# Kernel tuning notes

Measured on AMD Instinct MI355X. Metric: run time of the kernel, lower is better.

The kernel has to match this reference:

```python
import jax, jax.numpy as jnp
import numpy as np

def setup_inputs() -> dict:
    key = jax.random.key(0)
    ks = jax.random.split(key, 6)
    ch, cr = 256, 32  # cr = ch // 8
    B, H, W = 4, 64, 64
    sc = 1.0 / np.sqrt(ch)
    return {
        "inputs": jax.random.normal(ks[0], (B, H, W, ch), jnp.float32),
        "Wf": jax.random.normal(ks[1], (ch, cr), jnp.float32) * sc,
        "bf": jnp.zeros((cr,), jnp.float32),
        "Wg": jax.random.normal(ks[2], (ch, cr), jnp.float32) * sc,
        "bg": jnp.zeros((cr,), jnp.float32),
        "Wh": jax.random.normal(ks[3], (ch, cr), jnp.float32) * sc,
        "bh": jnp.zeros((cr,), jnp.float32),
        "Wv": jax.random.normal(ks[4], (cr, ch), jnp.float32) * (1.0 / np.sqrt(cr)),
        "bv": jnp.zeros((ch,), jnp.float32),
        "gamma": jnp.zeros((1,), jnp.float32),
    }

def reference(inputs, Wf, bf, Wg, bg, Wh, bh, Wv, bv, gamma):
    B, H, W, C = inputs.shape
    x = inputs.reshape(B, H * W, C)  # [B, N, C]
    f = x @ Wf + bf  # [B, N, cr] (keys)
    g = x @ Wg + bg  # [B, N, cr] (queries)
    h = x @ Wh + bh  # [B, N, cr] (values)
    s = jnp.einsum('bnk,bmk->bnm', g, f)  # [B, N, N]
    beta = jax.nn.softmax(s, axis=-1)
    v = jnp.einsum('bnm,bmk->bnk', beta, h)  # [B, N, cr]
    o = v @ Wv + bv  # [B, N, C]
    out = gamma * o + x
    return out.reshape(B, H, W, C)
```

## Files before the change

kernel.cpp:

```cpp
#include <hip/hip_runtime.h>

#define B_SZ  4
#define N_TOK 4096
#define CH    256
#define CR    32
#define SEG   512
#define KT    64
#define NITER (SEG / KT)
#define LOG2E 1.44269504f
#define SHIFT2 (12.0f * 1.44269504f)

typedef __attribute__((ext_vector_type(8))) short bf16x8;
typedef __attribute__((ext_vector_type(4))) float f32x4;

__device__ inline ushort f2bf(float x) {
    uint u = __float_as_uint(x);
    u += 0x7fff + ((u >> 16) & 1);
    return (ushort)(u >> 16);
}
__device__ inline uint pk2bf(float a, float b) {
    return __builtin_amdgcn_perm(__float_as_uint(b), __float_as_uint(a), 0x07060302);
}
__device__ inline float fast_exp2(float x) {
#if __has_builtin(__builtin_amdgcn_exp2f)
    return __builtin_amdgcn_exp2f(x);
#else
    return exp2f(x);
#endif
}

__global__ __launch_bounds__(256) void prep_kernel(
    const float* __restrict__ Wf, const float* __restrict__ Wg,
    const float* __restrict__ Wh, const float* __restrict__ Wv,
    ushort* __restrict__ wft, ushort* __restrict__ wgt,
    ushort* __restrict__ wht, ushort* __restrict__ wvt)
{
    int t = threadIdx.x, blk = blockIdx.x;
    if (blk < 3) {
        const float* W  = (blk == 0) ? Wf : (blk == 1) ? Wg : Wh;
        ushort*      Wt = (blk == 0) ? wft : (blk == 1) ? wgt : wht;
        int j = t & 31, half = t >> 5;
        ushort tmp[32];
        #pragma unroll
        for (int kk = 0; kk < 32; ++kk)
            tmp[kk] = f2bf(W[(half * 32 + kk) * CR + j]);
        ushort* dst = Wt + (size_t)j * CH + half * 32;
        #pragma unroll
        for (int k8 = 0; k8 < 4; ++k8)
            *(bf16x8*)(dst + k8 * 8) = *(bf16x8*)&tmp[k8 * 8];
    } else {
        ushort tmp[32];
        #pragma unroll
        for (int k = 0; k < CR; ++k) tmp[k] = f2bf(Wv[k * CH + t]);
        ushort* dst = wvt + (size_t)t * CR;
        #pragma unroll
        for (int k8 = 0; k8 < 4; ++k8)
            *(bf16x8*)(dst + k8 * 8) = *(bf16x8*)&tmp[k8 * 8];
    }
}

__global__ __launch_bounds__(256) void proj_kernel(
    const float* __restrict__ x,
    const ushort* __restrict__ wft, const ushort* __restrict__ wgt, const ushort* __restrict__ wht,
    const float* __restrict__ bf_, const float* __restrict__ bg, const float* __restrict__ bh,
    ushort* __restrict__ fo, ushort* __restrict__ go, ushort* __restrict__ hto)
{
    __shared__ f32x4 accx[3][6][64];
    int t  = threadIdx.x;
    int wv = t >> 6, L = t & 63, nl = L & 15, Q = L >> 4;
    int row_t = blockIdx.x * 16;
    int b = row_t >> 12, tok0 = row_t & 4095;

    const float* xrow = x + (size_t)(row_t + nl) * CH;
    f32x4 A[6];
    #pragma unroll
    for (int i = 0; i < 6; ++i) A[i] = (f32x4){0.f, 0.f, 0.f, 0.f};

    #pragma unroll
    for (int c2 = 0; c2 < 2; ++c2) {
        int off = wv * 64 + c2 * 32 + Q * 8;
        float4 lo = *(const float4*)(xrow + off);
        float4 hi = *(const float4*)(xrow + off + 4);
        bf16x8 xa;
        xa[0] = (short)f2bf(lo.x); xa[1] = (short)f2bf(lo.y);
        xa[2] = (short)f2bf(lo.z); xa[3] = (short)f2bf(lo.w);
        xa[4] = (short)f2bf(hi.x); xa[5] = (short)f2bf(hi.y);
        xa[6] = (short)f2bf(hi.z); xa[7] = (short)f2bf(hi.w);

        bf16x8 wf0 = *(const bf16x8*)(wft + (size_t)nl * CH + off);
        bf16x8 wf1 = *(const bf16x8*)(wft + (size_t)(16 + nl) * CH + off);
        bf16x8 wg0 = *(const bf16x8*)(wgt + (size_t)nl * CH + off);
        bf16x8 wg1 = *(const bf16x8*)(wgt + (size_t)(16 + nl) * CH + off);
        bf16x8 wh0 = *(const bf16x8*)(wht + (size_t)nl * CH + off);
        bf16x8 wh1 = *(const bf16x8*)(wht + (size_t)(16 + nl) * CH + off);

        A[0] = __builtin_amdgcn_mfma_f32_16x16x32_bf16(xa, wf0, A[0], 0, 0, 0);
        A[1] = __builtin_amdgcn_mfma_f32_16x16x32_bf16(xa, wf1, A[1], 0, 0, 0);
        A[2] = __builtin_amdgcn_mfma_f32_16x16x32_bf16(xa, wg0, A[2], 0, 0, 0);
        A[3] = __builtin_amdgcn_mfma_f32_16x16x32_bf16(xa, wg1, A[3], 0, 0, 0);
        A[4] = __builtin_amdgcn_mfma_f32_16x16x32_bf16(wh0, xa, A[4], 0, 0, 0);
        A[5] = __builtin_amdgcn_mfma_f32_16x16x32_bf16(wh1, xa, A[5], 0, 0, 0);
    }

    if (wv > 0) {
        #pragma unroll
        for (int i = 0; i < 6; ++i) accx[wv - 1][i][L] = A[i];
    }
    __syncthreads();
    if (wv == 0) {
        #pragma unroll
        for (int i = 0; i < 6; ++i) {
            f32x4 s0 = accx[0][i][L], s1 = accx[1][i][L], s2 = accx[2][i][L];
            A[i] = A[i] + s0 + s1 + s2;
        }
        float bF0 = bf_[nl], bF1 = bf_[16 + nl];
        float bG0 = bg[nl] * LOG2E, bG1 = bg[16 + nl] * LOG2E;
        #pragma unroll
        for (int r = 0; r < 4; ++r) {
            size_t ro = (size_t)(row_t + Q * 4 + r) * CR;
            fo[ro + nl]      = f2bf(A[0][r] + bF0);
            fo[ro + 16 + nl] = f2bf(A[1][r] + bF1);
            go[ro + nl]      = f2bf(fmaf(A[2][r], LOG2E, bG0));
            go[ro + 16 + nl] = f2bf(fmaf(A[3][r], LOG2E, bG1));
        }
        ushort* hb = hto + (size_t)b * CR * N_TOK + tok0 + nl;
        #pragma unroll
        for (int r = 0; r < 4; ++r) {
            int ch = Q * 4 + r;
            hb[(size_t)ch * N_TOK]        = f2bf(A[4][r] + bh[ch]);
            hb[(size_t)(16 + ch) * N_TOK] = f2bf(A[5][r] + bh[16 + ch]);
        }
    }
}

__global__ __launch_bounds__(512, 4) void attn_kernel(
    const ushort* __restrict__ f, const ushort* __restrict__ g,
    const ushort* __restrict__ ht, const ushort* __restrict__ wvt,
    const float* __restrict__ bv, const float* __restrict__ gamma,
    const float* __restrict__ x, float* __restrict__ out)
{
    __shared__ unsigned long long smem_raw[38912 / 8];
    ushort (*pls)[32][76]  = (ushort (*)[32][76])smem_raw;
    float  (*obuf)[32][33] = (float (*)[32][33])smem_raw;
    float  (*lbuf)[32]     = (float (*)[32])((char*)smem_raw + 33792);
    ushort (*oc)[48]       = (ushort (*)[48])((char*)smem_raw + 34816);

    int t  = threadIdx.x;
    int wv = t >> 6;
    int L  = t & 63;
    int nl = L & 15;
    int Q  = L >> 4;
    int b  = blockIdx.x >> 7;
    int q0 = (blockIdx.x & 127) * 32;

    const ushort* fb  = f  + (size_t)b * N_TOK * CR;
    const ushort* htb = ht + (size_t)b * CR * N_TOK;

    bf16x8 gB0 = *(const bf16x8*)(g + ((size_t)b * N_TOK + q0 + nl) * CR + Q * 8);
    bf16x8 gB1 = *(const bf16x8*)(g + ((size_t)b * N_TOK + q0 + 16 + nl) * CR + Q * 8);

    f32x4 acc00 = {0,0,0,0}, acc01 = {0,0,0,0};
    f32x4 acc10 = {0,0,0,0}, acc11 = {0,0,0,0};
    const f32x4 zf = {0,0,0,0};
    float lsum0 = 0.f, lsum1 = 0.f;

    int key0 = wv * SEG;
    bf16x8 Ac0 = *(const bf16x8*)(fb + (size_t)(key0 +  0 + nl) * CR + Q * 8);
    bf16x8 Ac1 = *(const bf16x8*)(fb + (size_t)(key0 + 16 + nl) * CR + Q * 8);
    bf16x8 Ac2 = *(const bf16x8*)(fb + (size_t)(key0 + 32 + nl) * CR + Q * 8);
    bf16x8 Ac3 = *(const bf16x8*)(fb + (size_t)(key0 + 48 + nl) * CR + Q * 8);

    #pragma unroll 2
    for (int it = 0; it < NITER; ++it) {
        int kc = wv * SEG + it * KT;
        const ushort* hk = htb + (size_t)nl * N_TOK + kc;
        bf16x8 b00 = *(const bf16x8*)(hk + Q * 8);
        bf16x8 b01 = *(const bf16x8*)(hk + (size_t)16 * N_TOK + Q * 8);
        bf16x8 b10 = *(const bf16x8*)(hk + 32 + Q * 8);
        bf16x8 b11 = *(const bf16x8*)(hk + (size_t)16 * N_TOK + 32 + Q * 8);
        int kn = wv * SEG + ((it + 1 < NITER) ? it + 1 : 0) * KT;
        const ushort* fn = fb + (size_t)kn * CR;
        bf16x8 An0 = *(const bf16x8*)(fn + (size_t)( 0 + nl) * CR + Q * 8);
        bf16x8 An1 = *(const bf16x8*)(fn + (size_t)(16 + nl) * CR + Q * 8);
        bf16x8 An2 = *(const bf16x8*)(fn + (size_t)(32 + nl) * CR + Q * 8);
        bf16x8 An3 = *(const bf16x8*)(fn + (size_t)(48 + nl) * CR + Q * 8);

        f32x4 s00 = __builtin_amdgcn_mfma_f32_16x16x32_bf16(Ac0, gB0, zf, 0, 0, 0);
        f32x4 s01 = __builtin_amdgcn_mfma_f32_16x16x32_bf16(Ac1, gB0, zf, 0, 0, 0);
        f32x4 s02 = __builtin_amdgcn_mfma_f32_16x16x32_bf16(Ac2, gB0, zf, 0, 0, 0);
        f32x4 s03 = __builtin_amdgcn_mfma_f32_16x16x32_bf16(Ac3, gB0, zf, 0, 0, 0);
        f32x4 s10 = __builtin_amdgcn_mfma_f32_16x16x32_bf16(Ac0, gB1, zf, 0, 0, 0);
        f32x4 s11 = __builtin_amdgcn_mfma_f32_16x16x32_bf16(Ac1, gB1, zf, 0, 0, 0);
        f32x4 s12 = __builtin_amdgcn_mfma_f32_16x16x32_bf16(Ac2, gB1, zf, 0, 0, 0);
        f32x4 s13 = __builtin_amdgcn_mfma_f32_16x16x32_bf16(Ac3, gB1, zf, 0, 0, 0);

        #pragma unroll
        for (int qh = 0; qh < 2; ++qh) {
            f32x4 v0 = qh ? s10 : s00, v1 = qh ? s11 : s01;
            f32x4 v2 = qh ? s12 : s02, v3 = qh ? s13 : s03;
            int row = qh * 16 + nl;
            float p0 = fast_exp2(v0[0]-SHIFT2), p1 = fast_exp2(v0[1]-SHIFT2);
            float p2 = fast_exp2(v0[2]-SHIFT2), p3 = fast_exp2(v0[3]-SHIFT2);
            float s4 = ((p0+p1)+(p2+p3));
            uint2 w; w.x = pk2bf(p0,p1); w.y = pk2bf(p2,p3);
            *(uint2*)&pls[wv][row][ 0 + Q * 4] = w;
            p0 = fast_exp2(v1[0]-SHIFT2); p1 = fast_exp2(v1[1]-SHIFT2);
            p2 = fast_exp2(v1[2]-SHIFT2); p3 = fast_exp2(v1[3]-SHIFT2);
            s4 += ((p0+p1)+(p2+p3));
            w.x = pk2bf(p0,p1); w.y = pk2bf(p2,p3);
            *(uint2*)&pls[wv][row][16 + Q * 4] = w;
            p0 = fast_exp2(v2[0]-SHIFT2); p1 = fast_exp2(v2[1]-SHIFT2);
            p2 = fast_exp2(v2[2]-SHIFT2); p3 = fast_exp2(v2[3]-SHIFT2);
            s4 += ((p0+p1)+(p2+p3));
            w.x = pk2bf(p0,p1); w.y = pk2bf(p2,p3);
            *(uint2*)&pls[wv][row][32 + Q * 4] = w;
            p0 = fast_exp2(v3[0]-SHIFT2); p1 = fast_exp2(v3[1]-SHIFT2);
            p2 = fast_exp2(v3[2]-SHIFT2); p3 = fast_exp2(v3[3]-SHIFT2);
            s4 += ((p0+p1)+(p2+p3));
            w.x = pk2bf(p0,p1); w.y = pk2bf(p2,p3);
            *(uint2*)&pls[wv][row][48 + Q * 4] = w;
            if (qh) lsum1 += s4; else lsum0 += s4;
        }

        bf16x8 aP00 = *(const bf16x8*)&pls[wv][     nl][ 0 + Q * 8];
        bf16x8 aP01 = *(const bf16x8*)&pls[wv][     nl][32 + Q * 8];
        bf16x8 aP10 = *(const bf16x8*)&pls[wv][16 + nl][ 0 + Q * 8];
        bf16x8 aP11 = *(const bf16x8*)&pls[wv][16 + nl][32 + Q * 8];

        acc00 = __builtin_amdgcn_mfma_f32_16x16x32_bf16(aP00, b00, acc00, 0, 0, 0);
        acc01 = __builtin_amdgcn_mfma_f32_16x16x32_bf16(aP00, b01, acc01, 0, 0, 0);
        acc10 = __builtin_amdgcn_mfma_f32_16x16x32_bf16(aP10, b00, acc10, 0, 0, 0);
        acc11 = __builtin_amdgcn_mfma_f32_16x16x32_bf16(aP10, b01, acc11, 0, 0, 0);
        acc00 = __builtin_amdgcn_mfma_f32_16x16x32_bf16(aP01, b10, acc00, 0, 0, 0);
        acc01 = __builtin_amdgcn_mfma_f32_16x16x32_bf16(aP01, b11, acc01, 0, 0, 0);
        acc10 = __builtin_amdgcn_mfma_f32_16x16x32_bf16(aP11, b10, acc10, 0, 0, 0);
        acc11 = __builtin_amdgcn_mfma_f32_16x16x32_bf16(aP11, b11, acc11, 0, 0, 0);

        Ac0 = An0; Ac1 = An1; Ac2 = An2; Ac3 = An3;
    }

    lsum0 += __shfl_xor(lsum0, 16); lsum0 += __shfl_xor(lsum0, 32);
    lsum1 += __shfl_xor(lsum1, 16); lsum1 += __shfl_xor(lsum1, 32);

    __syncthreads();
    #pragma unroll
    for (int r = 0; r < 4; ++r) {
        obuf[wv][     Q * 4 + r][nl]      = acc00[r];
        obuf[wv][     Q * 4 + r][16 + nl] = acc01[r];
        obuf[wv][16 + Q * 4 + r][nl]      = acc10[r];
        obuf[wv][16 + Q * 4 + r][16 + nl] = acc11[r];
    }
    if (L < 16) { lbuf[wv][nl] = lsum0; lbuf[wv][16 + nl] = lsum1; }
    __syncthreads();

    {
        int ch = t & 31, qb = t >> 5;
        #pragma unroll
        for (int qq = qb; qq < 32; qq += 16) {
            float s = 0.f, Lq = 0.f;
            #pragma unroll
            for (int w = 0; w < 8; ++w) { s += obuf[w][qq][ch]; Lq += lbuf[w][qq]; }
            oc[qq][ch] = f2bf(s / Lq);
        }
    }
    __syncthreads();

    bf16x8 aO0 = *(const bf16x8*)&oc[     nl][Q * 8];
    bf16x8 aO1 = *(const bf16x8*)&oc[16 + nl][Q * 8];
    float gm = gamma[0];
    const float* xb = x   + ((size_t)b * N_TOK + q0) * CH;
    float*       ob = out + ((size_t)b * N_TOK + q0) * CH;
    #pragma unroll
    for (int i = 0; i < 2; ++i) {
        int nb = wv * 2 + i;
        bf16x8 bW = *(const bf16x8*)(wvt + (size_t)(nb * 16 + nl) * CR + Q * 8);
        f32x4 d0 = __builtin_amdgcn_mfma_f32_16x16x32_bf16(aO0, bW, zf, 0, 0, 0);
        f32x4 d1 = __builtin_amdgcn_mfma_f32_16x16x32_bf16(aO1, bW, zf, 0, 0, 0);
        int c = nb * 16 + nl;
        float bvc = bv[c];
        #pragma unroll
        for (int r = 0; r < 4; ++r) {
            int qa = Q * 4 + r;
            ob[qa * CH + c]        = fmaf(gm, d0[r] + bvc, xb[qa * CH + c]);
            ob[(16 + qa) * CH + c] = fmaf(gm, d1[r] + bvc, xb[(16 + qa) * CH + c]);
        }
    }
}

extern "C" void kernel_launch(void* const* d_in, const int* in_sizes, int n_in,
                              void* d_out, int out_size, void* d_ws, size_t ws_size,
                              hipStream_t stream) {
    const float* x     = (const float*)d_in[0];
    const float* Wf    = (const float*)d_in[1];
    const float* bf_   = (const float*)d_in[2];
    const float* Wg    = (const float*)d_in[3];
    const float* bg    = (const float*)d_in[4];
    const float* Wh    = (const float*)d_in[5];
    const float* bh    = (const float*)d_in[6];
    const float* Wv    = (const float*)d_in[7];
    const float* bv    = (const float*)d_in[8];
    const float* gamma = (const float*)d_in[9];
    float* out = (float*)d_out;

    const size_t T = (size_t)B_SZ * N_TOK * CR;
    ushort* fo  = (ushort*)d_ws;
    ushort* go  = fo + T;
    ushort* hto = go + T;
    ushort* wvt = hto + T;
    ushort* wft = wvt + CH * CR;
    ushort* wgt = wft + CH * CR;
    ushort* wht = wgt + CH * CR;

    prep_kernel<<<4, 256, 0, stream>>>(Wf, Wg, Wh, Wv, wft, wgt, wht, wvt);
    proj_kernel<<<B_SZ * N_TOK / 16, 256, 0, stream>>>(x, wft, wgt, wht, bf_, bg, bh, fo, go, hto);
    attn_kernel<<<B_SZ * (N_TOK / 32), 512, 0, stream>>>(fo, go, hto, wvt, bv, gamma, x, out);
}
```

Measured before the change: 121.8 us.

## Software-pipeline QK and PV stages, compute row sums via MFMA, swizzle blocks

The attention loop is restructured so the QK^T scores and exponentials for the next key tile are computed before the PV MFMAs of the current tile. This overlaps the exp/pack work of one tile with the matrix work of another, and the PV MFMAs are raised to higher priority with s_setprio. Softmax row sums now come from extra MFMAs against a vector of ones, replacing the per-lane VALU adds and cross-lane shuffles. The constant exponent shift is removed and block indices are swizzled across batches to change cache locality. The trade-offs are more MFMA work, more live registers, and a higher overflow risk in the unshifted exponent if scores grow large.

```diff
diff --git a/kernel.cpp b/kernel.cpp
--- a/kernel.cpp
+++ b/kernel.cpp
@@ -8,7 +8,6 @@
 #define KT    64
 #define NITER (SEG / KT)
 #define LOG2E 1.44269504f
-#define SHIFT2 (12.0f * 1.44269504f)
 
 typedef __attribute__((ext_vector_type(8))) short bf16x8;
 typedef __attribute__((ext_vector_type(4))) float f32x4;
@@ -27,6 +26,13 @@
 #else
     return exp2f(x);
 #endif
+}
+
+__device__ inline void exp_pack_store(const f32x4 v, ushort* dst) {
+    float p0 = fast_exp2(v[0]), p1 = fast_exp2(v[1]);
+    float p2 = fast_exp2(v[2]), p3 = fast_exp2(v[3]);
+    uint2 w; w.x = pk2bf(p0, p1); w.y = pk2bf(p2, p3);
+    *(uint2*)dst = w;
 }
 
 __global__ __launch_bounds__(256) void prep_kernel(
@@ -150,8 +156,10 @@
     int L  = t & 63;
     int nl = L & 15;
     int Q  = L >> 4;
-    int b  = blockIdx.x >> 7;
-    int q0 = (blockIdx.x & 127) * 32;
+    int bid = blockIdx.x;
+    int swz = (bid & 7) * 64 + (bid >> 3);
+    int b  = swz >> 7;
+    int q0 = (swz & 127) * 32;
 
     const ushort* fb  = f  + (size_t)b * N_TOK * CR;
     const ushort* htb = ht + (size_t)b * CR * N_TOK;
@@ -161,72 +169,83 @@
 
     f32x4 acc00 = {0,0,0,0}, acc01 = {0,0,0,0};
     f32x4 acc10 = {0,0,0,0}, acc11 = {0,0,0,0};
+    f32x4 accS0 = {0,0,0,0}, accS1 = {0,0,0,0};
     const f32x4 zf = {0,0,0,0};
-    float lsum0 = 0.f, lsum1 = 0.f;
+
+    bf16x8 ones;
+    #pragma unroll
+    for (int i = 0; i < 8; ++i) ones[i] = (short)0x3F80;
 
     int key0 = wv * SEG;
-    bf16x8 Ac0 = *(const bf16x8*)(fb + (size_t)(key0 +  0 + nl) * CR + Q * 8);
-    bf16x8 Ac1 = *(const bf16x8*)(fb + (size_t)(key0 + 16 + nl) * CR + Q * 8);
-    bf16x8 Ac2 = *(const bf16x8*)(fb + (size_t)(key0 + 32 + nl) * CR + Q * 8);
-    bf16x8 Ac3 = *(const bf16x8*)(fb + (size_t)(key0 + 48 + nl) * CR + Q * 8);
-
-    #pragma unroll 2
+
+    bf16x8 Ap0 = *(const bf16x8*)(fb + (size_t)(key0 +  0 + nl) * CR + Q * 8);
+    bf16x8 Ap1 = *(const bf16x8*)(fb + (size_t)(key0 + 16 + nl) * CR + Q * 8);
+    bf16x8 Ap2 = *(const bf16x8*)(fb + (size_t)(key0 + 32 + nl) * CR + Q * 8);
+    bf16x8 Ap3 = *(const bf16x8*)(fb + (size_t)(key0 + 48 + nl) * CR + Q * 8);
+    bf16x8 An0 = *(const bf16x8*)(fb + (size_t)(key0 + KT +  0 + nl) * CR + Q * 8);
+    bf16x8 An1 = *(const bf16x8*)(fb + (size_t)(key0 + KT + 16 + nl) * CR + Q * 8);
+    bf16x8 An2 = *(const bf16x8*)(fb + (size_t)(key0 + KT + 32 + nl) * CR + Q * 8);
+    bf16x8 An3 = *(const bf16x8*)(fb + (size_t)(key0 + KT + 48 + nl) * CR + Q * 8);
+
+    {
+        f32x4 s0 = __builtin_amdgcn_mfma_f32_16x16x32_bf16(Ap0, gB0, zf, 0, 0, 0);
+        f32x4 s1 = __builtin_amdgcn_mfma_f32_16x16x32_bf16(Ap1, gB0, zf, 0, 0, 0);
+        f32x4 s2 = __builtin_amdgcn_mfma_f32_16x16x32_bf16(Ap2, gB0, zf, 0, 0, 0);
+        f32x4 s3 = __builtin_amdgcn_mfma_f32_16x16x32_bf16(Ap3, gB0, zf, 0, 0, 0);
+        exp_pack_store(s0, &pls[wv][nl][ 0 + Q * 4]);
+        exp_pack_store(s1, &pls[wv][nl][16 + Q * 4]);
+        exp_pack_store(s2, &pls[wv][nl][32 + Q * 4]);
+        exp_pack_store(s3, &pls[wv][nl][48 + Q * 4]);
+        s0 = __builtin_amdgcn_mfma_f32_16x16x32_bf16(Ap0, gB1, zf, 0, 0, 0);
+        s1 = __builtin_amdgcn_mfma_f32_16x16x32_bf16(Ap1, gB1, zf, 0, 0, 0);
+        s2 = __builtin_amdgcn_mfma_f32_16x16x32_bf16(Ap2, gB1, zf, 0, 0, 0);
+        s3 = __builtin_amdgcn_mfma_f32_16x16x32_bf16(Ap3, gB1, zf, 0, 0, 0);
+        exp_pack_store(s0, &pls[wv][16 + nl][ 0 + Q * 4]);
+        exp_pack_store(s1, &pls[wv][16 + nl][16 + Q * 4]);
+        exp_pack_store(s2, &pls[wv][16 + nl][32 + Q * 4]);
+        exp_pack_store(s3, &pls[wv][16 + nl][48 + Q * 4]);
+    }
+
+    #pragma unroll
     for (int it = 0; it < NITER; ++it) {
-        int kc = wv * SEG + it * KT;
+        bf16x8 aP00 = *(const bf16x8*)&pls[wv][     nl][ 0 + Q * 8];
+        bf16x8 aP01 = *(const bf16x8*)&pls[wv][     nl][32 + Q * 8];
+        bf16x8 aP10 = *(const bf16x8*)&pls[wv][16 + nl][ 0 + Q * 8];
+        bf16x8 aP11 = *(const bf16x8*)&pls[wv][16 + nl][32 + Q * 8];
+        int kc = key0 + it * KT;
         const ushort* hk = htb + (size_t)nl * N_TOK + kc;
         bf16x8 b00 = *(const bf16x8*)(hk + Q * 8);
         bf16x8 b01 = *(const bf16x8*)(hk + (size_t)16 * N_TOK + Q * 8);
         bf16x8 b10 = *(const bf16x8*)(hk + 32 + Q * 8);
         bf16x8 b11 = *(const bf16x8*)(hk + (size_t)16 * N_TOK + 32 + Q * 8);
-        int kn = wv * SEG + ((it + 1 < NITER) ? it + 1 : 0) * KT;
-        const ushort* fn = fb + (size_t)kn * CR;
-        bf16x8 An0 = *(const bf16x8*)(fn + (size_t)( 0 + nl) * CR + Q * 8);
-        bf16x8 An1 = *(const bf16x8*)(fn + (size_t)(16 + nl) * CR + Q * 8);
-        bf16x8 An2 = *(const bf16x8*)(fn + (size_t)(32 + nl) * CR + Q * 8);
-        bf16x8 An3 = *(const bf16x8*)(fn + (size_t)(48 + nl) * CR + Q * 8);
-
-        f32x4 s00 = __builtin_amdgcn_mfma_f32_16x16x32_bf16(Ac0, gB0, zf, 0, 0, 0);
-        f32x4 s01 = __builtin_amdgcn_mfma_f32_16x16x32_bf16(Ac1, gB0, zf, 0, 0, 0);
-        f32x4 s02 = __builtin_amdgcn_mfma_f32_16x16x32_bf16(Ac2, gB0, zf, 0, 0, 0);
-        f32x4 s03 = __builtin_amdgcn_mfma_f32_16x16x32_bf16(Ac3, gB0, zf, 0, 0, 0);
-        f32x4 s10 = __builtin_amdgcn_mfma_f32_16x16x32_bf16(Ac0, gB1, zf, 0, 0, 0);
-        f32x4 s11 = __builtin_amdgcn_mfma_f32_16x16x32_bf16(Ac1, gB1, zf, 0, 0, 0);
-        f32x4 s12 = __builtin_amdgcn_mfma_f32_16x16x32_bf16(Ac2, gB1, zf, 0, 0, 0);
-        f32x4 s13 = __builtin_amdgcn_mfma_f32_16x16x32_bf16(Ac3, gB1, zf, 0, 0, 0);
-
-        #pragma unroll
-        for (int qh = 0; qh < 2; ++qh) {
-            f32x4 v0 = qh ? s10 : s00, v1 = qh ? s11 : s01;
-            f32x4 v2 = qh ? s12 : s02, v3 = qh ? s13 : s03;
-            int row = qh * 16 + nl;
-            float p0 = fast_exp2(v0[0]-SHIFT2), p1 = fast_exp2(v0[1]-SHIFT2);
-            float p2 = fast_exp2(v0[2]-SHIFT2), p3 = fast_exp2(v0[3]-SHIFT2);
-            float s4 = ((p0+p1)+(p2+p3));
-            uint2 w; w.x = pk2bf(p0,p1); w.y = pk2bf(p2,p3);
-            *(uint2*)&pls[wv][row][ 0 + Q * 4] = w;
-            p0 = fast_exp2(v1[0]-SHIFT2); p1 = fast_exp2(v1[1]-SHIFT2);
-            p2 = fast_exp2(v1[2]-SHIFT2); p3 = fast_exp2(v1[3]-SHIFT2);
-            s4 += ((p0+p1)+(p2+p3));
-            w.x = pk2bf(p0,p1); w.y = pk2bf(p2,p3);
-            *(uint2*)&pls[wv][row][16 + Q * 4] = w;
-            p0 = fast_exp2(v2[0]-SHIFT2); p1 = fast_exp2(v2[1]-SHIFT2);
-            p2 = fast_exp2(v2[2]-SHIFT2); p3 = fast_exp2(v2[3]-SHIFT2);
-            s4 += ((p0+p1)+(p2+p3));
-            w.x = pk2bf(p0,p1); w.y = pk2bf(p2,p3);
-            *(uint2*)&pls[wv][row][32 + Q * 4] = w;
-            p0 = fast_exp2(v3[0]-SHIFT2); p1 = fast_exp2(v3[1]-SHIFT2);
-            p2 = fast_exp2(v3[2]-SHIFT2); p3 = fast_exp2(v3[3]-SHIFT2);
-            s4 += ((p0+p1)+(p2+p3));
-            w.x = pk2bf(p0,p1); w.y = pk2bf(p2,p3);
-            *(uint2*)&pls[wv][row][48 + Q * 4] = w;
-            if (qh) lsum1 += s4; else lsum0 += s4;
-        }
-
-        bf16x8 aP00 = *(const bf16x8*)&pls[wv][     nl][ 0 + Q * 8];
-        bf16x8 aP01 = *(const bf16x8*)&pls[wv][     nl][32 + Q * 8];
-        bf16x8 aP10 = *(const bf16x8*)&pls[wv][16 + nl][ 0 + Q * 8];
-        bf16x8 aP11 = *(const bf16x8*)&pls[wv][16 + nl][32 + Q * 8];
-
+
+        if (it + 1 < NITER) {
+            int kn = key0 + ((it + 2 < NITER) ? it + 2 : 0) * KT;
+            const ushort* fn = fb + (size_t)kn * CR;
+            bf16x8 Nx0 = *(const bf16x8*)(fn + (size_t)( 0 + nl) * CR + Q * 8);
+            bf16x8 Nx1 = *(const bf16x8*)(fn + (size_t)(16 + nl) * CR + Q * 8);
+            bf16x8 Nx2 = *(const bf16x8*)(fn + (size_t)(32 + nl) * CR + Q * 8);
+            bf16x8 Nx3 = *(const bf16x8*)(fn + (size_t)(48 + nl) * CR + Q * 8);
+            f32x4 s0 = __builtin_amdgcn_mfma_f32_16x16x32_bf16(An0, gB0, zf, 0, 0, 0);
+            f32x4 s1 = __builtin_amdgcn_mfma_f32_16x16x32_bf16(An1, gB0, zf, 0, 0, 0);
+            f32x4 s2 = __builtin_amdgcn_mfma_f32_16x16x32_bf16(An2, gB0, zf, 0, 0, 0);
+            f32x4 s3 = __builtin_amdgcn_mfma_f32_16x16x32_bf16(An3, gB0, zf, 0, 0, 0);
+            exp_pack_store(s0, &pls[wv][nl][ 0 + Q * 4]);
+            exp_pack_store(s1, &pls[wv][nl][16 + Q * 4]);
+            exp_pack_store(s2, &pls[wv][nl][32 + Q * 4]);
+            exp_pack_store(s3, &pls[wv][nl][48 + Q * 4]);
+            s0 = __builtin_amdgcn_mfma_f32_16x16x32_bf16(An0, gB1, zf, 0, 0, 0);
+            s1 = __builtin_amdgcn_mfma_f32_16x16x32_bf16(An1, gB1, zf, 0, 0, 0);
+            s2 = __builtin_amdgcn_mfma_f32_16x16x32_bf16(An2, gB1, zf, 0, 0, 0);
+            s3 = __builtin_amdgcn_mfma_f32_16x16x32_bf16(An3, gB1, zf, 0, 0, 0);
+            exp_pack_store(s0, &pls[wv][16 + nl][ 0 + Q * 4]);
+            exp_pack_store(s1, &pls[wv][16 + nl][16 + Q * 4]);
+            exp_pack_store(s2, &pls[wv][16 + nl][32 + Q * 4]);
+            exp_pack_store(s3, &pls[wv][16 + nl][48 + Q * 4]);
+            An0 = Nx0; An1 = Nx1; An2 = Nx2; An3 = Nx3;
+        }
+
+        __builtin_amdgcn_s_setprio(1);
         acc00 = __builtin_amdgcn_mfma_f32_16x16x32_bf16(aP00, b00, acc00, 0, 0, 0);
         acc01 = __builtin_amdgcn_mfma_f32_16x16x32_bf16(aP00, b01, acc01, 0, 0, 0);
         acc10 = __builtin_amdgcn_mfma_f32_16x16x32_bf16(aP10, b00, acc10, 0, 0, 0);
@@ -235,12 +254,12 @@
         acc01 = __builtin_amdgcn_mfma_f32_16x16x32_bf16(aP01, b11, acc01, 0, 0, 0);
         acc10 = __builtin_amdgcn_mfma_f32_16x16x32_bf16(aP11, b10, acc10, 0, 0, 0);
         acc11 = __builtin_amdgcn_mfma_f32_16x16x32_bf16(aP11, b11, acc11, 0, 0, 0);
-
-        Ac0 = An0; Ac1 = An1; Ac2 = An2; Ac3 = An3;
-    }
-
-    lsum0 += __shfl_xor(lsum0, 16); lsum0 += __shfl_xor(lsum0, 32);
-    lsum1 += __shfl_xor(lsum1, 16); lsum1 += __shfl_xor(lsum1, 32);
+        accS0 = __builtin_amdgcn_mfma_f32_16x16x32_bf16(aP00, ones, accS0, 0, 0, 0);
+        accS0 = __builtin_amdgcn_mfma_f32_16x16x32_bf16(aP01, ones, accS0, 0, 0, 0);
+        accS1 = __builtin_amdgcn_mfma_f32_16x16x32_bf16(aP10, ones, accS1, 0, 0, 0);
+        accS1 = __builtin_amdgcn_mfma_f32_16x16x32_bf16(aP11, ones, accS1, 0, 0, 0);
+        __builtin_amdgcn_s_setprio(0);
+    }
 
     __syncthreads();
     #pragma unroll
@@ -250,7 +269,13 @@
         obuf[wv][16 + Q * 4 + r][nl]      = acc10[r];
         obuf[wv][16 + Q * 4 + r][16 + nl] = acc11[r];
     }
-    if (L < 16) { lbuf[wv][nl] = lsum0; lbuf[wv][16 + nl] = lsum1; }
+    if (nl == 0) {
+        #pragma unroll
+        for (int r = 0; r < 4; ++r) {
+            lbuf[wv][     Q * 4 + r] = accS0[r];
+            lbuf[wv][16 + Q * 4 + r] = accS1[r];
+        }
+    }
     __syncthreads();
 
     {
```

Result: slower. 131.2 us (+7.7%).
